# Kernel tuning notes

Measured on AMD Instinct MI355X. Metric: run time of the kernel, lower is better.

## Reference

```python
import math
import jax, jax.numpy as jnp
import numpy as np

V, D, H, L, F, S, B = 32000, 768, 12, 6, 3072, 2048, 4
DK = D // H


def setup_inputs() -> dict:
    key = jax.random.key(0)
    ks = jax.random.split(key, 16)
    sc = 0.02
    n = jax.random.normal
    inp = {
        "input_ids": jax.random.randint(ks[0], (B, S), 0, V, dtype=jnp.int64)
        if jax.config.jax_enable_x64 else jax.random.randint(ks[0], (B, S), 0, V, dtype=jnp.int32),
        "emb": n(ks[1], (V, D), jnp.float32) * sc,
        "Wq": n(ks[2], (L, D, D), jnp.float32) * sc, "bq": jnp.zeros((L, D), jnp.float32),
        "Wk": n(ks[3], (L, D, D), jnp.float32) * sc, "bk": jnp.zeros((L, D), jnp.float32),
        "Wv": n(ks[4], (L, D, D), jnp.float32) * sc, "bv": jnp.zeros((L, D), jnp.float32),
        "Wo": n(ks[5], (L, D, D), jnp.float32) * sc, "bo": jnp.zeros((L, D), jnp.float32),
        "W1": n(ks[6], (L, D, F), jnp.float32) * sc, "b1": jnp.zeros((L, F), jnp.float32),
        "W2": n(ks[7], (L, F, D), jnp.float32) * sc, "b2": jnp.zeros((L, D), jnp.float32),
        "gamma": jnp.ones((L, D), jnp.float32), "beta": jnp.zeros((L, D), jnp.float32),
    }
    return inp


def _pos_encoding(seq_len, d):
    pos = jnp.arange(seq_len, dtype=jnp.float32)[:, None]                  # [S,1]
    div = jnp.exp(jnp.arange(0, d, 2, dtype=jnp.float32) * (-math.log(10000.0) / d))
    ang = pos * div                                                        # [S,D/2]
    return jnp.stack([jnp.sin(ang), jnp.cos(ang)], axis=-1).reshape(seq_len, d)


def _layernorm(x, g, b, eps=1e-5):
    mu = x.mean(-1, keepdims=True)
    var = ((x - mu) ** 2).mean(-1, keepdims=True)
    return (x - mu) * jax.lax.rsqrt(var + eps) * g + b


def _forward(input_ids, emb, Wq, bq, Wk, bk, Wv, bv, Wo, bo, W1, b1, W2, b2, gamma, beta):
    mask = (input_ids != 1)[:, None, None, :]                              # [B,1,1,S]
    x = emb[input_ids] + _pos_encoding(input_ids.shape[1], emb.shape[1])   # [B,S,D]

    def layer(x, p):
        wq, bq_, wk, bk_, wv, bv_, wo, bo_, w1, b1_, w2, b2_, g, bt = p
        def heads(h):  # [B,S,D] -> [B,H,S,DK]
            return h.reshape(B, S, H, DK).transpose(0, 2, 1, 3)
        q = heads(x @ wq + bq_)
        k = heads(x @ wk + bk_)
        v = heads(x @ wv + bv_)
        scores = jnp.einsum("bhqd,bhkd->bhqk", q, k) / math.sqrt(DK)
        scores = jnp.where(mask, scores, -1e9)
        attn = jax.nn.softmax(scores, axis=-1)
        o = jnp.einsum("bhqk,bhkd->bhqd", attn, v)
        o = o.transpose(0, 2, 1, 3).reshape(B, S, D) @ wo + bo_
        x1 = _layernorm(x + o, g, bt)
        ff = jax.nn.relu(x1 @ w1 + b1_) @ w2 + b2_
        return _layernorm(x1 + ff, g, bt), None  # same norm params reused (as in source)

    x, _ = jax.lax.scan(layer, x, (Wq, bq, Wk, bk, Wv, bv, Wo, bo, W1, b1, W2, b2, gamma, beta))
    return x.mean(axis=1)                                                  # [B,D]


def reference(input_ids, emb, Wq, bq, Wk, bk, Wv, bv, Wo, bo, W1, b1, W2, b2, gamma, beta):
    return _forward(input_ids, emb, Wq, bq, Wk, bk, Wv, bv, Wo, bo, W1, b1, W2, b2, gamma, beta)
```

## Files before the change

### kernel.cpp

```cpp
#include <hip/hip_runtime.h>
#include <hip/hip_bf16.h>
#include <math.h>

typedef unsigned short u16;
typedef unsigned long long u64;
using bf16x8 = __attribute__((ext_vector_type(8))) short;
using f32x4  = __attribute__((ext_vector_type(4))) float;

static constexpr int kD = 768;
static constexpr int kH = 12;
static constexpr int kL = 6;
static constexpr int kF = 3072;
static constexpr int kS = 2048;
static constexpr int kB = 4;
static constexpr int kQW = 2304;
static constexpr int kNT = kB * kS;

static constexpr float kQScale = 0.18033688011112043f;

__device__ __forceinline__ u16 f2bf(float f) {
    return __bfloat16_as_ushort(__float2bfloat16(f));
}
__device__ __forceinline__ float b2f(u16 u) {
    return __uint_as_float((unsigned)u << 16);
}
__device__ __forceinline__ unsigned cvtpk(float a, float b) {
    unsigned d;
    asm volatile("v_cvt_pk_bf16_f32 %0, %1, %2" : "=v"(d) : "v"(a), "v"(b));
    return d;
}
__device__ __forceinline__ float exp2fast(float x) {
#if __has_builtin(__builtin_amdgcn_exp2f)
    return __builtin_amdgcn_exp2f(x);
#else
    return __expf(x * 0.6931471805599453f);
#endif
}

__device__ __forceinline__ void gload16(const void* g, void* l) {
    auto gp = reinterpret_cast<const __attribute__((address_space(1))) unsigned int*>(
        reinterpret_cast<uintptr_t>(g));
    auto lp = reinterpret_cast<__attribute__((address_space(3))) unsigned int*>(
        reinterpret_cast<uintptr_t>(l));
    __builtin_amdgcn_global_load_lds(gp, lp, 16, 0, 0);
}

__global__ __launch_bounds__(256) void embed_pe(
    const int* __restrict__ ids, const float* __restrict__ emb,
    u16* __restrict__ xbf)
{
    const int t = blockIdx.x;
    const int s = t & (kS - 1);
    const int id = ids[t];
#pragma unroll
    for (int j = 0; j < 3; ++j) {
        const int d = threadIdx.x + (j << 8);
        const float i2 = (float)((d >> 1) << 1);
        const float dv = __expf(i2 * (-9.210340371976184f / 768.f));
        const float ang = (float)s * dv;
        const float pe = (d & 1) ? cosf(ang) : sinf(ang);
        xbf[(size_t)t * kD + d] = f2bf(emb[(size_t)id * kD + d] + pe);
    }
}

__global__ __launch_bounds__(256) void embed_pe_f32(
    const int* __restrict__ ids, const float* __restrict__ emb,
    float* __restrict__ x)
{
    const int t = blockIdx.x;
    const int s = t & (kS - 1);
    const int id = ids[t];
#pragma unroll
    for (int j = 0; j < 3; ++j) {
        const int d = threadIdx.x + (j << 8);
        const float i2 = (float)((d >> 1) << 1);
        const float dv = __expf(i2 * (-9.210340371976184f / 768.f));
        const float ang = (float)s * dv;
        const float pe = (d & 1) ? cosf(ang) : sinf(ang);
        x[(size_t)t * kD + d] = emb[(size_t)id * kD + d] + pe;
    }
}

__global__ __launch_bounds__(64) void mk_maskbits(const int* __restrict__ ids,
                                                  u64* __restrict__ mbits)
{
    const int w = blockIdx.x;
    const int lane = threadIdx.x;
    const u64 m = __ballot(ids[(size_t)w * 64 + lane] != 1);
    if (lane == 0) mbits[w] = m;
}

__global__ __launch_bounds__(256) void bias_build(
    const float* __restrict__ bq, const float* __restrict__ bk,
    const float* __restrict__ bv, const float* __restrict__ bo,
    const float* __restrict__ b1, const float* __restrict__ b2,
    float* __restrict__ ba)
{
    const int i = blockIdx.x * 256 + threadIdx.x;
    if (i >= 6 * 6912) return;
    const int l = i / 6912, p = i % 6912;
    float v;
    if      (p < 768)  v = bq[l * 768 + p] * kQScale;
    else if (p < 1536) v = bk[l * 768 + p - 768];
    else if (p < 2304) v = bv[l * 768 + p - 1536];
    else if (p < 3072) v = bo[l * 768 + p - 2304];
    else if (p < 6144) v = b1[(size_t)l * 3072 + p - 3072];
    else               v = b2[l * 768 + p - 6144];
    ba[i] = v;
}

static constexpr size_t OFF_WO = (size_t)2304 * 768;
static constexpr size_t OFF_W1 = OFF_WO + (size_t)768 * 768;
static constexpr size_t OFF_W2 = OFF_W1 + (size_t)3072 * 768;
static constexpr size_t WARENA_E = OFF_W2 + (size_t)768 * 3072;

__global__ __launch_bounds__(256) void cvt_all(
    const float* __restrict__ Wq, const float* __restrict__ Wk,
    const float* __restrict__ Wv, const float* __restrict__ Wo,
    const float* __restrict__ W1, const float* __restrict__ W2,
    u16* __restrict__ wa)
{
    __shared__ float T[64][68];
    const int t = blockIdx.x;
    const float* S; u16* Dp; int Nsrc, Kdst, srow0, scol0; float sc = 1.f;
    if (t < 432) {
        const int ni = t % 36, ki = t / 36;
        const int ng = ni * 64;
        const int sel = ng / 768;
        scol0 = ng % 768; srow0 = ki * 64;
        S = (sel == 0) ? Wq : (sel == 1) ? Wk : Wv;
        if (sel == 0) sc = kQScale;
        Nsrc = 768; Kdst = 768;
        Dp = wa + (size_t)ng * 768 + srow0;
    } else if (t < 576) {
        const int tt = t - 432; const int ni = tt % 12, ki = tt / 12;
        scol0 = ni * 64; srow0 = ki * 64;
        S = Wo; Nsrc = 768; Kdst = 768;
        Dp = wa + OFF_WO + (size_t)(ni * 64) * 768 + srow0;
    } else if (t < 1152) {
        const int tt = t - 576; const int ni = tt % 48, ki = tt / 48;
        scol0 = ni * 64; srow0 = ki * 64;
        S = W1; Nsrc = 3072; Kdst = 768;
        Dp = wa + OFF_W1 + (size_t)(ni * 64) * 768 + srow0;
    } else {
        const int tt = t - 1152; const int ni = tt % 12, ki = tt / 12;
        scol0 = ni * 64; srow0 = ki * 64;
        S = W2; Nsrc = 768; Kdst = 3072;
        Dp = wa + OFF_W2 + (size_t)(ni * 64) * 3072 + srow0;
    }
    const int tid = threadIdx.x;
#pragma unroll
    for (int i = 0; i < 4; ++i) {
        const int idx = tid + (i << 8);
        const int kr = idx >> 4;
        const int nc = (idx & 15) << 2;
        const float4 v = *(const float4*)(S + (size_t)(srow0 + kr) * Nsrc + scol0 + nc);
        T[kr][nc] = v.x; T[kr][nc + 1] = v.y; T[kr][nc + 2] = v.z; T[kr][nc + 3] = v.w;
    }
    __syncthreads();
#pragma unroll
    for (int i = 0; i < 4; ++i) {
        const int idx = tid + (i << 8);
        const int nr = idx >> 4;
        const int kc = (idx & 15) << 2;
        ushort4 o;
        o.x = f2bf(T[kc][nr] * sc);     o.y = f2bf(T[kc + 1][nr] * sc);
        o.z = f2bf(T[kc + 2][nr] * sc); o.w = f2bf(T[kc + 3][nr] * sc);
        *(ushort4*)(Dp + (size_t)nr * Kdst + kc) = o;
    }
}

__global__ __launch_bounds__(512, 1) void gemm256(
    const u16* __restrict__ A, const u16* __restrict__ Bt,
    const float* __restrict__ bias, void* __restrict__ Cv,
    u16* __restrict__ vTp, int M, int N, int K, int mode)
{
    __shared__ u16 As[3][8192];
    __shared__ u16 Bs[3][8192];
    const int tid = threadIdx.x;
    const int l = tid & 63;
    const int lo = l & 15, hi = l >> 4;
    const int w = tid >> 6, wr = w >> 2, wc = w & 3;

    int brow = blockIdx.x, bcol = blockIdx.y;
    const int gx = gridDim.x;
    if ((gx & 7) == 0) {
        const int id = blockIdx.y * gx + blockIdx.x;
        const int xcd = id & 7, idx = id >> 3;
        const int rpx = gx >> 3;
        brow = xcd * rpx + (idx % rpx);
        bcol = idx / rpx;
    }
    const size_t row0 = (size_t)brow * 256;
    const size_t col0 = (size_t)bcol * 256;

    const int c0 = tid, c1 = tid + 512;
    const int r0 = c0 >> 2, g0 = (c0 & 3) ^ ((r0 >> 1) & 3);
    const int r1 = c1 >> 2, g1 = (c1 & 3) ^ ((r1 >> 1) & 3);
    const u16* a0 = A  + (row0 + r0) * K + g0 * 8;
    const u16* a1 = A  + (row0 + r1) * K + g1 * 8;
    const u16* b0 = Bt + (col0 + r0) * K + g0 * 8;
    const u16* b1 = Bt + (col0 + r1) * K + g1 * 8;

    f32x4 acc[8][4];
#pragma unroll
    for (int i = 0; i < 8; ++i)
#pragma unroll
        for (int j = 0; j < 4; ++j)
#pragma unroll
            for (int r = 0; r < 4; ++r) acc[i][j][r] = 0.f;

    int aoff[8], boff[4];
#pragma unroll
    for (int i = 0; i < 8; ++i) {
        const int ra = wr * 128 + i * 16 + lo;
        aoff[i] = ra * 32 + ((hi ^ ((ra >> 1) & 3)) << 3);
    }
#pragma unroll
    for (int j = 0; j < 4; ++j) {
        const int rb = wc * 64 + j * 16 + lo;
        boff[j] = rb * 32 + ((hi ^ ((rb >> 1) & 3)) << 3);
    }

    const int NT = K >> 5;
#pragma unroll
    for (int t = 0; t < 2; ++t) {
        const int k0 = t << 5;
        gload16(a0 + k0, As[t] + c0 * 8);
        gload16(a1 + k0, As[t] + c1 * 8);
        gload16(b0 + k0, Bs[t] + c0 * 8);
        gload16(b1 + k0, Bs[t] + c1 * 8);
    }

    int cur = 0;
    for (int t = 0; t < NT; ++t) {
        if (t + 1 < NT) {
            asm volatile("s_waitcnt vmcnt(8)" ::: "memory");
        } else {
            asm volatile("s_waitcnt vmcnt(0)" ::: "memory");
        }
        __builtin_amdgcn_s_barrier();
        if (t + 2 < NT) {
            const int k0 = (t + 2) << 5;
            const int nb = (cur + 2 >= 3) ? cur - 1 : cur + 2;
            gload16(a0 + k0, As[nb] + c0 * 8);
            gload16(a1 + k0, As[nb] + c1 * 8);
            gload16(b0 + k0, Bs[nb] + c0 * 8);
            gload16(b1 + k0, Bs[nb] + c1 * 8);
        }
        bf16x8 af[8], bfr[4];
#pragma unroll
        for (int i = 0; i < 8; ++i) af[i]  = *(const bf16x8*)&As[cur][aoff[i]];
#pragma unroll
        for (int j = 0; j < 4; ++j) bfr[j] = *(const bf16x8*)&Bs[cur][boff[j]];
        __builtin_amdgcn_s_setprio(1);
#pragma unroll
        for (int i = 0; i < 8; ++i)
#pragma unroll
            for (int j = 0; j < 4; ++j)
                acc[i][j] = __builtin_amdgcn_mfma_f32_16x16x32_bf16(
                    af[i], bfr[j], acc[i][j], 0, 0, 0);
        __builtin_amdgcn_s_setprio(0);
        cur = (cur + 1 == 3) ? 0 : cur + 1;
    }

    const bool vmode = (mode == 3) && (col0 >= 1536);
    if (vmode) {
#pragma unroll
        for (int i = 0; i < 8; ++i) {
            const size_t rbase = row0 + wr * 128 + i * 16 + hi * 4;
            const size_t tb = (rbase >> 6) * 64;
            const int k0 = (int)(rbase & 63);
            const int pos = (((k0 >> 2) & 3) << 3) + (((k0 >> 4) & 1) << 2)
                          + ((k0 >> 5) << 5);
#pragma unroll
            for (int j = 0; j < 4; ++j) {
                const size_t c = col0 + wc * 64 + j * 16 + lo;
                const float bs = bias[c];
                const size_t d = c - 1536;
                ushort4 o;
                o.x = f2bf(acc[i][j][0] + bs);
                o.y = f2bf(acc[i][j][1] + bs);
                o.z = f2bf(acc[i][j][2] + bs);
                o.w = f2bf(acc[i][j][3] + bs);
                *(ushort4*)(vTp + d * (size_t)M + tb + pos) = o;
            }
        }
        return;
    }

#pragma unroll
    for (int i = 0; i < 8; ++i) {
        const size_t rbase = row0 + wr * 128 + i * 16 + hi * 4;
#pragma unroll
        for (int j = 0; j < 4; ++j) {
            const size_t c = col0 + wc * 64 + j * 16 + lo;
            const float bs = bias[c];
#pragma unroll
            for (int r = 0; r < 4; ++r) {
                float v = acc[i][j][r] + bs;
                if (mode == 2) v = fmaxf(v, 0.f);
                ((u16*)Cv)[(rbase + r) * (size_t)N + c] = f2bf(v);
            }
        }
    }
}

__global__ __launch_bounds__(256) void gemm_bf16(
    const u16* __restrict__ A, const u16* __restrict__ Bt,
    const float* __restrict__ bias, void* __restrict__ Cv,
    u16* __restrict__ vTp, int M, int N, int K, int mode)
{
    __shared__ u16 As[2][4096];
    __shared__ u16 Bs[2][4096];
    const int tid = threadIdx.x;
    const int l = tid & 63;
    const int lo = l & 15, hi = l >> 4;
    const int w = tid >> 6, wr = w >> 1, wc = w & 1;

    int brow = blockIdx.x, bcol = blockIdx.y;
    const int gx = gridDim.x;
    if ((gx & 7) == 0) {
        const int id = blockIdx.y * gx + blockIdx.x;
        const int xcd = id & 7, idx = id >> 3;
        const int rpx = gx >> 3;
        brow = xcd * rpx + (idx % rpx);
        bcol = idx / rpx;
    }
    const size_t row0 = (size_t)brow * 128;
    const size_t col0 = (size_t)bcol * 128;

    const int c0 = tid, c1 = tid + 256;
    const int r0 = c0 >> 2, g0 = (c0 & 3) ^ ((r0 >> 1) & 3);
    const int r1 = c1 >> 2, g1 = (c1 & 3) ^ ((r1 >> 1) & 3);
    const u16* a0 = A  + (row0 + r0) * K + g0 * 8;
    const u16* a1 = A  + (row0 + r1) * K + g1 * 8;
    const u16* b0 = Bt + (col0 + r0) * K + g0 * 8;
    const u16* b1 = Bt + (col0 + r1) * K + g1 * 8;

    f32x4 acc[4][4];
#pragma unroll
    for (int i = 0; i < 4; ++i)
#pragma unroll
        for (int j = 0; j < 4; ++j)
#pragma unroll
            for (int r = 0; r < 4; ++r) acc[i][j][r] = 0.f;

    int aoff[4], boff[4];
#pragma unroll
    for (int i = 0; i < 4; ++i) {
        const int ra = wr * 64 + i * 16 + lo;
        aoff[i] = ra * 32 + ((hi ^ ((ra >> 1) & 3)) << 3);
        const int rb = wc * 64 + i * 16 + lo;
        boff[i] = rb * 32 + ((hi ^ ((rb >> 1) & 3)) << 3);
    }

    const int NT = K >> 5;
    gload16(a0, As[0] + c0 * 8);
    gload16(a1, As[0] + c1 * 8);
    gload16(b0, Bs[0] + c0 * 8);
    gload16(b1, Bs[0] + c1 * 8);

    int cur = 0;
    for (int t = 0; t < NT; ++t) {
        if (t + 1 < NT) {
            const int k0 = (t + 1) << 5;
            const int nb = cur ^ 1;
            gload16(a0 + k0, As[nb] + c0 * 8);
            gload16(a1 + k0, As[nb] + c1 * 8);
            gload16(b0 + k0, Bs[nb] + c0 * 8);
            gload16(b1 + k0, Bs[nb] + c1 * 8);
            asm volatile("s_waitcnt vmcnt(4)" ::: "memory");
        } else {
            asm volatile("s_waitcnt vmcnt(0)" ::: "memory");
        }
        __builtin_amdgcn_s_barrier();
        bf16x8 af[4], bfr[4];
#pragma unroll
        for (int i = 0; i < 4; ++i) af[i]  = *(const bf16x8*)&As[cur][aoff[i]];
#pragma unroll
        for (int j = 0; j < 4; ++j) bfr[j] = *(const bf16x8*)&Bs[cur][boff[j]];
#pragma unroll
        for (int i = 0; i < 4; ++i)
#pragma unroll
            for (int j = 0; j < 4; ++j)
                acc[i][j] = __builtin_amdgcn_mfma_f32_16x16x32_bf16(
                    af[i], bfr[j], acc[i][j], 0, 0, 0);
        asm volatile("s_waitcnt lgkmcnt(0)" ::: "memory");
        __builtin_amdgcn_sched_barrier(0);
        __builtin_amdgcn_s_barrier();
        cur ^= 1;
    }

#pragma unroll
    for (int i = 0; i < 4; ++i) {
        const size_t rbase = row0 + wr * 64 + i * 16 + hi * 4;
#pragma unroll
        for (int j = 0; j < 4; ++j) {
            const size_t c = col0 + wc * 64 + j * 16 + lo;
            const float bs = bias[c];
#pragma unroll
            for (int r = 0; r < 4; ++r) {
                float v = acc[i][j][r] + bs;
                if (mode == 2) v = fmaxf(v, 0.f);
                ((u16*)Cv)[(rbase + r) * (size_t)N + c] = f2bf(v);
            }
        }
    }
}

__global__ __launch_bounds__(512) void attn_mfma(
    const u16* __restrict__ QKV, const u16* __restrict__ vT,
    const u64* __restrict__ mbits, u16* __restrict__ O)
{
    __shared__ u16 Ks[2][4096];
    __shared__ u16 Vs[2][4096];

    const int tid = threadIdx.x, l = tid & 63, w = tid >> 6;
    const int lo = l & 15, hi = l >> 4;

    const int flat = blockIdx.x + 16 * (blockIdx.y + 12 * blockIdx.z);
    const int nf = (flat & 7) * 96 + (flat >> 3);
    const int qi = nf & 15;
    const int h  = (nf >> 4) % 12;
    const int b  = nf / 192;
    const int q0 = qi << 7;

    bf16x8 qf0, qf1;
    {
        const u16* qp = QKV + ((size_t)(b * kS + q0 + w * 16 + lo)) * kQW
                            + h * 64 + hi * 8;
        qf0 = *(const bf16x8*)qp;
        qf1 = *(const bf16x8*)(qp + 32);
    }

    const int rw = tid >> 3, sx = tid & 7, E = sx ^ (rw & 7);
    const u16* Kbase = QKV + (size_t)(b * kS) * kQW + 768 + h * 64;
    const u16* Vbase = vT + (size_t)(h * 64) * kNT + b * kS;

    f32x4 accO[4];
#pragma unroll
    for (int n = 0; n < 4; ++n)
#pragma unroll
        for (int r = 0; r < 4; ++r) accO[n][r] = 0.f;
    float m = -3.0e38f, lsum = 0.f;

    const int ksw = (lo & 7) << 3;
    constexpr int NTt = kS / 64;

    gload16(Kbase + (size_t)rw * kQW + E * 8, Ks[0] + tid * 8);
    gload16(Vbase + (size_t)rw * kNT + E * 8, Vs[0] + tid * 8);

    int cur = 0;
    for (int kt = 0; kt < NTt; ++kt) {
        asm volatile("s_waitcnt vmcnt(0)" ::: "memory");
        __syncthreads();

        if (kt + 1 < NTt) {
            const size_t kof = (size_t)((kt + 1) << 6) * kQW;
            const size_t vof = (size_t)((kt + 1) << 6);
            gload16(Kbase + kof + (size_t)rw * kQW + E * 8, Ks[cur ^ 1] + tid * 8);
            gload16(Vbase + (size_t)rw * kNT + vof + E * 8, Vs[cur ^ 1] + tid * 8);
        }

        f32x4 st[4];
        __builtin_amdgcn_s_setprio(1);
#pragma unroll
        for (int j = 0; j < 4; ++j) {
#pragma unroll
            for (int r = 0; r < 4; ++r) st[j][r] = 0.f;
            const int kb2 = (j * 16 + lo) * 64;
            const bf16x8 k0 = *(const bf16x8*)&Ks[cur][kb2 + ((hi * 8)      ^ ksw)];
            const bf16x8 k1 = *(const bf16x8*)&Ks[cur][kb2 + ((hi * 8 + 32) ^ ksw)];
            st[j] = __builtin_amdgcn_mfma_f32_16x16x32_bf16(k0, qf0, st[j], 0, 0, 0);
            st[j] = __builtin_amdgcn_mfma_f32_16x16x32_bf16(k1, qf1, st[j], 0, 0, 0);
        }
        __builtin_amdgcn_s_setprio(0);

        float rmax = st[0][0];
#pragma unroll
        for (int j = 0; j < 4; ++j)
#pragma unroll
            for (int r = 0; r < 4; ++r) rmax = fmaxf(rmax, st[j][r]);
        rmax = fmaxf(rmax, __shfl_xor(rmax, 16));
        rmax = fmaxf(rmax, __shfl_xor(rmax, 32));

        const bool skip = __all(rmax <= m + 11.0f);
        if (!skip) {
            const float mn = fmaxf(m, rmax);
            const float corr = exp2fast(m - mn);
            m = mn;
            lsum *= corr;
            float c2[4];
#pragma unroll
            for (int r = 0; r < 4; ++r) c2[r] = __shfl(corr, hi * 4 + r);
#pragma unroll
            for (int n = 0; n < 4; ++n)
#pragma unroll
                for (int r = 0; r < 4; ++r) accO[n][r] *= c2[r];
        }

#pragma unroll
        for (int j = 0; j < 4; ++j)
#pragma unroll
            for (int r = 0; r < 4; ++r) st[j][r] = exp2fast(st[j][r] - m);

        const u64 mb = mbits[b * 32 + kt];
        if (mb != ~0ull) {
#pragma unroll
            for (int j = 0; j < 4; ++j)
#pragma unroll
                for (int r = 0; r < 4; ++r)
                    if (!((mb >> (j * 16 + hi * 4 + r)) & 1)) st[j][r] = 0.f;
        }

        float ts = 0.f;
#pragma unroll
        for (int j = 0; j < 4; ++j)
#pragma unroll
            for (int r = 0; r < 4; ++r) ts += st[j][r];
        ts += __shfl_xor(ts, 16);
        ts += __shfl_xor(ts, 32);
        lsum += ts;

        union PU { unsigned u[4]; bf16x8 v; } p0, p1;
        p0.u[0] = cvtpk(st[0][0], st[0][1]); p0.u[1] = cvtpk(st[0][2], st[0][3]);
        p0.u[2] = cvtpk(st[1][0], st[1][1]); p0.u[3] = cvtpk(st[1][2], st[1][3]);
        p1.u[0] = cvtpk(st[2][0], st[2][1]); p1.u[1] = cvtpk(st[2][2], st[2][3]);
        p1.u[2] = cvtpk(st[3][0], st[3][1]); p1.u[3] = cvtpk(st[3][2], st[3][3]);

        __builtin_amdgcn_s_setprio(1);
#pragma unroll
        for (int n = 0; n < 4; ++n) {
            const int vb2 = (n * 16 + lo) * 64;
            const bf16x8 v0 = *(const bf16x8*)&Vs[cur][vb2 + ((hi * 8)      ^ ksw)];
            const bf16x8 v1 = *(const bf16x8*)&Vs[cur][vb2 + ((hi * 8 + 32) ^ ksw)];
            accO[n] = __builtin_amdgcn_mfma_f32_16x16x32_bf16(p0.v, v0, accO[n], 0, 0, 0);
            accO[n] = __builtin_amdgcn_mfma_f32_16x16x32_bf16(p1.v, v1, accO[n], 0, 0, 0);
        }
        __builtin_amdgcn_s_setprio(0);
        cur ^= 1;
    }

    float linv[4];
#pragma unroll
    for (int r = 0; r < 4; ++r) linv[r] = 1.f / __shfl(lsum, hi * 4 + r);
#pragma unroll
    for (int n = 0; n < 4; ++n)
#pragma unroll
        for (int r = 0; r < 4; ++r)
            O[((size_t)(b * kS + q0 + w * 16 + hi * 4 + r)) * kD
              + h * 64 + n * 16 + lo] = f2bf(accO[n][r] * linv[r]);
}

__global__ __launch_bounds__(256) void add_ln_bf(
    const u16* __restrict__ a, const u16* __restrict__ r,
    const float* __restrict__ g, const float* __restrict__ bt,
    u16* __restrict__ out)
{
    const int lane = threadIdx.x & 63;
    const size_t row = (size_t)blockIdx.x * 4 + (threadIdx.x >> 6);
    const ushort4* a4 = (const ushort4*)(a + row * kD);
    const ushort4* r4 = (const ushort4*)(r + row * kD);
    float v[3][4];
    float s = 0.f;
#pragma unroll
    for (int j = 0; j < 3; ++j) {
        const ushort4 av = a4[j * 64 + lane];
        const ushort4 rv = r4[j * 64 + lane];
        v[j][0] = b2f(av.x) + b2f(rv.x);
        v[j][1] = b2f(av.y) + b2f(rv.y);
        v[j][2] = b2f(av.z) + b2f(rv.z);
        v[j][3] = b2f(av.w) + b2f(rv.w);
        s += v[j][0] + v[j][1] + v[j][2] + v[j][3];
    }
#pragma unroll
    for (int off = 32; off; off >>= 1) s += __shfl_xor(s, off);
    const float mu = s * (1.f / 768.f);
    float vs = 0.f;
#pragma unroll
    for (int j = 0; j < 3; ++j)
#pragma unroll
        for (int e = 0; e < 4; ++e) {
            const float t0 = v[j][e] - mu;
            vs = fmaf(t0, t0, vs);
        }
#pragma unroll
    for (int off = 32; off; off >>= 1) vs += __shfl_xor(vs, off);
    const float rstd = rsqrtf(vs * (1.f / 768.f) + 1e-5f);
    const float4* g4 = (const float4*)g;
    const float4* b4 = (const float4*)bt;
#pragma unroll
    for (int j = 0; j < 3; ++j) {
        const float4 gv = g4[j * 64 + lane];
        const float4 bv = b4[j * 64 + lane];
        ushort4 o;
        o.x = f2bf((v[j][0] - mu) * rstd * gv.x + bv.x);
        o.y = f2bf((v[j][1] - mu) * rstd * gv.y + bv.y);
        o.z = f2bf((v[j][2] - mu) * rstd * gv.z + bv.z);
        o.w = f2bf((v[j][3] - mu) * rstd * gv.w + bv.w);
        ((ushort4*)(out + row * kD))[j * 64 + lane] = o;
    }
}

__global__ __launch_bounds__(192) void mean_part_bf(
    const u16* __restrict__ x, float* __restrict__ mred)
{
    const int c = blockIdx.x, b = blockIdx.y;
    const int d = threadIdx.x * 4;
    const u16* base = x + ((size_t)b * kS + c * 32) * kD + d;
    float s0 = 0.f, s1 = 0.f, s2 = 0.f, s3 = 0.f;
#pragma unroll 8
    for (int t = 0; t < 32; ++t) {
        const ushort4 u = *(const ushort4*)(base + (size_t)t * kD);
        s0 += b2f(u.x); s1 += b2f(u.y); s2 += b2f(u.z); s3 += b2f(u.w);
    }
    float4 o; o.x = s0; o.y = s1; o.z = s2; o.w = s3;
    *(float4*)(mred + ((size_t)b * 64 + c) * kD + d) = o;
}

__global__ __launch_bounds__(256) void mean_fin(
    const float* __restrict__ mred, float* __restrict__ out)
{
    const int d = blockIdx.x * 256 + threadIdx.x;
    const int b = blockIdx.y;
    float s = 0.f;
#pragma unroll
    for (int c = 0; c < 64; ++c) s += mred[((size_t)b * 64 + c) * kD + d];
    out[b * kD + d] = s * (1.f / 2048.f);
}

__global__ __launch_bounds__(256) void add_ln_f32(
    const float* __restrict__ a, const float* __restrict__ r,
    const float* __restrict__ g, const float* __restrict__ bt,
    float* __restrict__ out)
{
    const int lane = threadIdx.x & 63;
    const size_t row = (size_t)blockIdx.x * 4 + (threadIdx.x >> 6);
    const float4* a4 = (const float4*)(a + row * kD);
    const float4* r4 = (const float4*)(r + row * kD);
    float4 v[3];
    float s = 0.f;
#pragma unroll
    for (int j = 0; j < 3; ++j) {
        const float4 av = a4[j * 64 + lane];
        const float4 rv = r4[j * 64 + lane];
        v[j].x = av.x + rv.x; v[j].y = av.y + rv.y;
        v[j].z = av.z + rv.z; v[j].w = av.w + rv.w;
        s += v[j].x + v[j].y + v[j].z + v[j].w;
    }
#pragma unroll
    for (int off = 32; off; off >>= 1) s += __shfl_xor(s, off);
    const float mu = s * (1.f / 768.f);
    float vs = 0.f;
#pragma unroll
    for (int j = 0; j < 3; ++j) {
        float t0 = v[j].x - mu, t1 = v[j].y - mu, t2 = v[j].z - mu, t3 = v[j].w - mu;
        vs = fmaf(t0, t0, fmaf(t1, t1, fmaf(t2, t2, fmaf(t3, t3, vs))));
    }
#pragma unroll
    for (int off = 32; off; off >>= 1) vs += __shfl_xor(vs, off);
    const float rstd = rsqrtf(vs * (1.f / 768.f) + 1e-5f);
    const float4* g4 = (const float4*)g;
    const float4* b4 = (const float4*)bt;
#pragma unroll
    for (int j = 0; j < 3; ++j) {
        const float4 gv = g4[j * 64 + lane];
        const float4 bv = b4[j * 64 + lane];
        float4 o;
        o.x = (v[j].x - mu) * rstd * gv.x + bv.x;
        o.y = (v[j].y - mu) * rstd * gv.y + bv.y;
        o.z = (v[j].z - mu) * rstd * gv.z + bv.z;
        o.w = (v[j].w - mu) * rstd * gv.w + bv.w;
        ((float4*)(out + row * kD))[j * 64 + lane] = o;
    }
}

__global__ __launch_bounds__(256) void mean_s(
    const float* __restrict__ x, float* __restrict__ out)
{
    const int d = blockIdx.x * 256 + threadIdx.x;
    const int b = blockIdx.y;
    float s = 0.f;
    for (int t = 0; t < kS; ++t) s += x[((size_t)b * kS + t) * kD + d];
    out[b * kD + d] = s * (1.f / 2048.f);
}

__global__ __launch_bounds__(256) void gemm_f32(
    const float* __restrict__ A, const float* __restrict__ W,
    const float* __restrict__ bias, float* __restrict__ C,
    int M, int N, int K, int relu)
{
    __shared__ float As[16][68];
    __shared__ float Bs[16][68];
    const int tid = threadIdx.x;
    const int row0 = blockIdx.x << 6;
    const int col0 = blockIdx.y << 6;
    const int tx = tid & 15, ty = tid >> 4;
    const int ar = tid >> 2;
    const int ak = (tid & 3) << 2;
    const int bk = tid >> 4;
    const int bc = (tid & 15) << 2;
    float acc[4][4] = {};
    const float* Ap = A + (size_t)(row0 + ar) * K + ak;
    const float* Wp = W + (size_t)bk * N + col0 + bc;
    for (int k0 = 0; k0 < K; k0 += 16) {
        const float4 a4 = *(const float4*)(Ap + k0);
        const float4 b4 = *(const float4*)(Wp + (size_t)k0 * N);
        __syncthreads();
        As[ak + 0][ar] = a4.x; As[ak + 1][ar] = a4.y;
        As[ak + 2][ar] = a4.z; As[ak + 3][ar] = a4.w;
        *(float4*)&Bs[bk][bc] = b4;
        __syncthreads();
#pragma unroll
        for (int kk = 0; kk < 16; ++kk) {
            const float4 av = *(const float4*)&As[kk][ty << 2];
            const float4 bv = *(const float4*)&Bs[kk][tx << 2];
            const float aa[4] = {av.x, av.y, av.z, av.w};
            const float bb[4] = {bv.x, bv.y, bv.z, bv.w};
#pragma unroll
            for (int i = 0; i < 4; ++i)
#pragma unroll
                for (int j = 0; j < 4; ++j)
                    acc[i][j] = fmaf(aa[i], bb[j], acc[i][j]);
        }
    }
#pragma unroll
    for (int i = 0; i < 4; ++i) {
        const int row = row0 + (ty << 2) + i;
#pragma unroll
        for (int j = 0; j < 4; ++j) {
            const int col = col0 + (tx << 2) + j;
            float v = acc[i][j] + bias[col];
            if (relu) v = fmaxf(v, 0.f);
            C[(size_t)row * N + col] = v;
        }
    }
}

__global__ __launch_bounds__(256) void attn_fused(
    const float* __restrict__ Q, const float* __restrict__ Km,
    const float* __restrict__ Vm, const int* __restrict__ ids,
    float* __restrict__ O)
{
    __shared__ float Ksf[64 * 64];
    __shared__ float Vtf[64 * 64];
    __shared__ float Qs[16][64];
    __shared__ float Psf[4][4][64];
    const int tid = threadIdx.x;
    const int w = tid >> 6;
    const int lane = tid & 63;
    const int h = blockIdx.y, b = blockIdx.z;
    const int qrow0 = blockIdx.x << 4;
    {
        const int r = tid >> 4;
        const int c4 = tid & 15;
        const float4 q4 = *(const float4*)(
            Q + ((size_t)(b * kS + qrow0 + r)) * kD + h * 64 + (c4 << 2));
        Qs[r][(c4 << 2) + 0] = q4.x * 0.125f;
        Qs[r][(c4 << 2) + 1] = q4.y * 0.125f;
        Qs[r][(c4 << 2) + 2] = q4.z * 0.125f;
        Qs[r][(c4 << 2) + 3] = q4.w * 0.125f;
    }
    float m[4], lsum[4], o[4];
#pragma unroll
    for (int r = 0; r < 4; ++r) { m[r] = -3.0e38f; lsum[r] = 0.f; o[r] = 0.f; }
    for (int kt = 0; kt < kS / 64; ++kt) {
        __syncthreads();
#pragma unroll
        for (int i = 0; i < 4; ++i) {
            const int lin = tid + (i << 8);
            const int row = lin >> 4;
            const int s4 = lin & 15;
            const size_t gro = ((size_t)(b * kS + (kt << 6) + row)) * kD + h * 64 + (s4 << 2);
            const float4 k4 = *(const float4*)(Km + gro);
            ((float4*)Ksf)[(row << 4) + (s4 ^ (row & 7))] = k4;
            const float4 v4 = *(const float4*)(Vm + gro);
            const int ksl = row >> 2, ke = row & 3;
            const int d0 = s4 << 2;
            Vtf[(d0 + 0) * 64 + ((ksl ^ ((d0 + 0) & 7)) << 2) + ke] = v4.x;
            Vtf[(d0 + 1) * 64 + ((ksl ^ ((d0 + 1) & 7)) << 2) + ke] = v4.y;
            Vtf[(d0 + 2) * 64 + ((ksl ^ ((d0 + 2) & 7)) << 2) + ke] = v4.z;
            Vtf[(d0 + 3) * 64 + ((ksl ^ ((d0 + 3) & 7)) << 2) + ke] = v4.w;
        }
        __syncthreads();
        const bool masked = (ids[(size_t)b * kS + (kt << 6) + lane] == 1);
        float scr[4] = {0.f, 0.f, 0.f, 0.f};
#pragma unroll
        for (int i16 = 0; i16 < 16; ++i16) {
            const float4 kv = ((const float4*)Ksf)[(lane << 4) + (i16 ^ (lane & 7))];
#pragma unroll
            for (int r = 0; r < 4; ++r) {
                const float4 qv = *(const float4*)&Qs[(w << 2) + r][i16 << 2];
                scr[r] = fmaf(kv.x, qv.x, fmaf(kv.y, qv.y,
                          fmaf(kv.z, qv.z, fmaf(kv.w, qv.w, scr[r]))));
            }
        }
#pragma unroll
        for (int r = 0; r < 4; ++r) {
            float sm = masked ? -3.0e38f : scr[r];
#pragma unroll
            for (int off = 32; off; off >>= 1) sm = fmaxf(sm, __shfl_xor(sm, off));
            const float mn = fmaxf(m[r], sm);
            const float cr = __expf(m[r] - mn);
            const float pv = masked ? 0.f : __expf(scr[r] - mn);
            float ps = pv;
#pragma unroll
            for (int off = 32; off; off >>= 1) ps += __shfl_xor(ps, off);
            lsum[r] = lsum[r] * cr + ps;
            o[r] *= cr;
            m[r] = mn;
            Psf[w][r][lane] = pv;
        }
#pragma unroll
        for (int i16 = 0; i16 < 16; ++i16) {
            const float4 vv = ((const float4*)Vtf)[(lane << 4) + (i16 ^ (lane & 7))];
#pragma unroll
            for (int r = 0; r < 4; ++r) {
                const float4 pv = *(const float4*)&Psf[w][r][i16 << 2];
                o[r] = fmaf(pv.x, vv.x, fmaf(pv.y, vv.y,
                        fmaf(pv.z, vv.z, fmaf(pv.w, vv.w, o[r]))));
            }
        }
    }
#pragma unroll
    for (int r = 0; r < 4; ++r)
        O[((size_t)(b * kS + qrow0 + (w << 2) + r)) * kD + h * 64 + lane] =
            o[r] / lsum[r];
}

extern "C" void kernel_launch(void* const* d_in, const int* in_sizes, int n_in,
                              void* d_out, int out_size, void* d_ws, size_t ws_size,
                              hipStream_t stream)
{
    const int*   ids   = (const int*)  d_in[0];
    const float* emb   = (const float*)d_in[1];
    const float* Wq    = (const float*)d_in[2];
    const float* bq    = (const float*)d_in[3];
    const float* Wk    = (const float*)d_in[4];
    const float* bk    = (const float*)d_in[5];
    const float* Wv    = (const float*)d_in[6];
    const float* bv    = (const float*)d_in[7];
    const float* Wo    = (const float*)d_in[8];
    const float* bo    = (const float*)d_in[9];
    const float* W1    = (const float*)d_in[10];
    const float* b1    = (const float*)d_in[11];
    const float* W2    = (const float*)d_in[12];
    const float* b2    = (const float*)d_in[13];
    const float* gamma = (const float*)d_in[14];
    const float* beta  = (const float*)d_in[15];
    float* out = (float*)d_out;

    const size_t BUFE = (size_t)kB * kS * kD;
    const size_t WDD  = (size_t)kD * kD;
    const size_t WDF  = (size_t)kD * kF;
    const size_t HIDE = (size_t)kB * kS * kF;
    const int NTOK = kB * kS;

    const size_t NEED = BUFE * 2 * 4
                      + HIDE * 2
                      + WARENA_E * 2
                      + (size_t)6 * 6912 * 4
                      + 128 * 8
                      + (size_t)kB * 64 * kD * 4;

    if (ws_size >= NEED) {
        u16*   xb  = (u16*)d_ws;
        u16*   x1b = xb + BUFE;
        u16*   ao  = x1b + BUFE;
        u16*   ob  = ao + BUFE;
        u16*   sc  = ob + BUFE;
        u16*   vtb = sc + (size_t)NTOK * kQW;
        u16*   wa  = sc + HIDE;
        float* ba  = (float*)(wa + WARENA_E);
        u64*   mbt = (u64*)(ba + 6 * 6912);
        float* mrd = (float*)(mbt + 128);

        embed_pe<<<NTOK, 256, 0, stream>>>(ids, emb, xb);
        mk_maskbits<<<kB * kS / 64, 64, 0, stream>>>(ids, mbt);
        bias_build<<<(6 * 6912 + 255) / 256, 256, 0, stream>>>(
            bq, bk, bv, bo, b1, b2, ba);

        for (int l = 0; l < kL; ++l) {
            const size_t oDD = (size_t)l * WDD;
            const size_t oDF = (size_t)l * WDF;
            const float* bl = ba + (size_t)l * 6912;
            const float* gl  = gamma + (size_t)l * kD;
            const float* btl = beta  + (size_t)l * kD;

            cvt_all<<<1728, 256, 0, stream>>>(
                Wq + oDD, Wk + oDD, Wv + oDD, Wo + oDD, W1 + oDF, W2 + oDF, wa);

            gemm256<<<dim3(32, 9), 512, 0, stream>>>(
                xb, wa, bl, sc, vtb, NTOK, kQW, kD, 3);

            attn_mfma<<<dim3(kS / 128, kH, kB), 512, 0, stream>>>(
                sc, vtb, mbt, ao);

            gemm_bf16<<<dim3(64, 6), 256, 0, stream>>>(
                ao, wa + OFF_WO, bl + 2304, ob, nullptr, NTOK, kD, kD, 1);

            add_ln_bf<<<NTOK / 4, 256, 0, stream>>>(xb, ob, gl, btl, x1b);

            gemm256<<<dim3(32, 12), 512, 0, stream>>>(
                x1b, wa + OFF_W1, bl + 3072, sc, nullptr, NTOK, kF, kD, 2);
            gemm_bf16<<<dim3(64, 6), 256, 0, stream>>>(
                sc, wa + OFF_W2, bl + 6144, ob, nullptr, NTOK, kD, kF, 1);

            add_ln_bf<<<NTOK / 4, 256, 0, stream>>>(x1b, ob, gl, btl, xb);
        }

        mean_part_bf<<<dim3(64, kB), 192, 0, stream>>>(xb, mrd);
        mean_fin<<<dim3(kD / 256, kB), 256, 0, stream>>>(mrd, out);
        return;
    }

    if (ws_size < 5 * BUFE * sizeof(float)) return;
    float* xb = (float*)d_ws;
    float* kb = xb + BUFE;
    float* qb = kb + BUFE;
    float* vb = qb + BUFE;
    float* obf = vb + BUFE;
    float* hb = qb;

    embed_pe_f32<<<NTOK, 256, 0, stream>>>(ids, emb, xb);
    for (int l = 0; l < kL; ++l) {
        const size_t oDD = (size_t)l * WDD;
        const size_t oDF = (size_t)l * WDF;
        gemm_f32<<<dim3(NTOK / 64, kD / 64), 256, 0, stream>>>(
            xb, Wq + oDD, bq + (size_t)l * kD, qb, NTOK, kD, kD, 0);
        gemm_f32<<<dim3(NTOK / 64, kD / 64), 256, 0, stream>>>(
            xb, Wk + oDD, bk + (size_t)l * kD, kb, NTOK, kD, kD, 0);
        gemm_f32<<<dim3(NTOK / 64, kD / 64), 256, 0, stream>>>(
            xb, Wv + oDD, bv + (size_t)l * kD, vb, NTOK, kD, kD, 0);
        attn_fused<<<dim3(kS / 16, kH, kB), 256, 0, stream>>>(qb, kb, vb, ids, obf);
        gemm_f32<<<dim3(NTOK / 64, kD / 64), 256, 0, stream>>>(
            obf, Wo + oDD, bo + (size_t)l * kD, qb, NTOK, kD, kD, 0);
        add_ln_f32<<<NTOK / 4, 256, 0, stream>>>(xb, qb,
            gamma + (size_t)l * kD, beta + (size_t)l * kD, kb);
        for (int c = 0; c < 2; ++c) {
            const size_t ro = (size_t)c * 4096;
            gemm_f32<<<dim3(4096 / 64, kF / 64), 256, 0, stream>>>(
                kb + ro * kD, W1 + oDF, b1 + (size_t)l * kF, hb, 4096, kF, kD, 1);
            gemm_f32<<<dim3(4096 / 64, kD / 64), 256, 0, stream>>>(
                hb, W2 + oDF, b2 + (size_t)l * kD, obf + ro * kD, 4096, kD, kF, 0);
        }
        add_ln_f32<<<NTOK / 4, 256, 0, stream>>>(kb, obf,
            gamma + (size_t)l * kD, beta + (size_t)l * kD, xb);
    }
    mean_s<<<dim3(kD / 256, kB), 256, 0, stream>>>(xb, out);
}
```

Measured before the change: 1.612 ms.

## Shrink big GEMM tile to 128x256 with 256 threads, two blocks per CU

Replaces the 256x256, 512-thread, triple-buffered GEMM used for the QKV and FFN1 projections with a 128x256 tile, 256 threads and double buffering. Launch bounds allow two blocks per CU, and the grid doubles in the row dimension. The intent is more resident blocks per CU and better load balance across the GPU. The cost is lower per-block data reuse (B tiles are fetched twice as often in total) and a shallower prefetch pipeline with an extra barrier per k-step.

Result: faster. 1.521 ms (-5.6%).

```diff
diff --git a/kernel.cpp b/kernel.cpp
--- a/kernel.cpp
+++ b/kernel.cpp
@@ -170,17 +170,17 @@
     }
 }
 
-__global__ __launch_bounds__(512, 1) void gemm256(
+__global__ __launch_bounds__(256, 2) void gemm256b(
     const u16* __restrict__ A, const u16* __restrict__ Bt,
     const float* __restrict__ bias, void* __restrict__ Cv,
     u16* __restrict__ vTp, int M, int N, int K, int mode)
 {
-    __shared__ u16 As[3][8192];
-    __shared__ u16 Bs[3][8192];
+    __shared__ u16 As[2][4096];
+    __shared__ u16 Bs[2][8192];
     const int tid = threadIdx.x;
     const int l = tid & 63;
     const int lo = l & 15, hi = l >> 4;
-    const int w = tid >> 6, wr = w >> 2, wc = w & 3;
+    const int wc = tid >> 6;
 
     int brow = blockIdx.x, bcol = blockIdx.y;
     const int gx = gridDim.x;
@@ -191,16 +191,21 @@
         brow = xcd * rpx + (idx % rpx);
         bcol = idx / rpx;
     }
-    const size_t row0 = (size_t)brow * 256;
+    const size_t row0 = (size_t)brow * 128;
     const size_t col0 = (size_t)bcol * 256;
 
-    const int c0 = tid, c1 = tid + 512;
-    const int r0 = c0 >> 2, g0 = (c0 & 3) ^ ((r0 >> 1) & 3);
-    const int r1 = c1 >> 2, g1 = (c1 & 3) ^ ((r1 >> 1) & 3);
-    const u16* a0 = A  + (row0 + r0) * K + g0 * 8;
-    const u16* a1 = A  + (row0 + r1) * K + g1 * 8;
-    const u16* b0 = Bt + (col0 + r0) * K + g0 * 8;
-    const u16* b1 = Bt + (col0 + r1) * K + g1 * 8;
+    const int ca0 = tid, ca1 = tid + 256;
+    const int ra0 = ca0 >> 2, ga0 = (ca0 & 3) ^ ((ra0 >> 1) & 3);
+    const int ra1 = ca1 >> 2, ga1 = (ca1 & 3) ^ ((ra1 >> 1) & 3);
+    const u16* aP0 = A + (row0 + ra0) * K + ga0 * 8;
+    const u16* aP1 = A + (row0 + ra1) * K + ga1 * 8;
+    const u16* bP[4];
+#pragma unroll
+    for (int q = 0; q < 4; ++q) {
+        const int c = tid + (q << 8);
+        const int r = c >> 2, g = (c & 3) ^ ((r >> 1) & 3);
+        bP[q] = Bt + (col0 + r) * K + g * 8;
+    }
 
     f32x4 acc[8][4];
 #pragma unroll
@@ -213,7 +218,7 @@
     int aoff[8], boff[4];
 #pragma unroll
     for (int i = 0; i < 8; ++i) {
-        const int ra = wr * 128 + i * 16 + lo;
+        const int ra = i * 16 + lo;
         aoff[i] = ra * 32 + ((hi ^ ((ra >> 1) & 3)) << 3);
     }
 #pragma unroll
@@ -223,31 +228,26 @@
     }
 
     const int NT = K >> 5;
-#pragma unroll
-    for (int t = 0; t < 2; ++t) {
-        const int k0 = t << 5;
-        gload16(a0 + k0, As[t] + c0 * 8);
-        gload16(a1 + k0, As[t] + c1 * 8);
-        gload16(b0 + k0, Bs[t] + c0 * 8);
-        gload16(b1 + k0, Bs[t] + c1 * 8);
-    }
-
-    int cur = 0;
+    gload16(aP0, As[0] + ca0 * 8);
+    gload16(aP1, As[0] + ca1 * 8);
+#pragma unroll
+    for (int q = 0; q < 4; ++q) gload16(bP[q], Bs[0] + (tid + (q << 8)) * 8);
+
     for (int t = 0; t < NT; ++t) {
+        const int cur = t & 1;
         if (t + 1 < NT) {
-            asm volatile("s_waitcnt vmcnt(8)" ::: "memory");
+            const int k0 = (t + 1) << 5;
+            const int nb = cur ^ 1;
+            gload16(aP0 + k0, As[nb] + ca0 * 8);
+            gload16(aP1 + k0, As[nb] + ca1 * 8);
+#pragma unroll
+            for (int q = 0; q < 4; ++q)
+                gload16(bP[q] + k0, Bs[nb] + (tid + (q << 8)) * 8);
+            asm volatile("s_waitcnt vmcnt(6)" ::: "memory");
         } else {
             asm volatile("s_waitcnt vmcnt(0)" ::: "memory");
         }
         __builtin_amdgcn_s_barrier();
-        if (t + 2 < NT) {
-            const int k0 = (t + 2) << 5;
-            const int nb = (cur + 2 >= 3) ? cur - 1 : cur + 2;
-            gload16(a0 + k0, As[nb] + c0 * 8);
-            gload16(a1 + k0, As[nb] + c1 * 8);
-            gload16(b0 + k0, Bs[nb] + c0 * 8);
-            gload16(b1 + k0, Bs[nb] + c1 * 8);
-        }
         bf16x8 af[8], bfr[4];
 #pragma unroll
         for (int i = 0; i < 8; ++i) af[i]  = *(const bf16x8*)&As[cur][aoff[i]];
@@ -261,14 +261,16 @@
                 acc[i][j] = __builtin_amdgcn_mfma_f32_16x16x32_bf16(
                     af[i], bfr[j], acc[i][j], 0, 0, 0);
         __builtin_amdgcn_s_setprio(0);
-        cur = (cur + 1 == 3) ? 0 : cur + 1;
+        asm volatile("s_waitcnt lgkmcnt(0)" ::: "memory");
+        __builtin_amdgcn_sched_barrier(0);
+        __builtin_amdgcn_s_barrier();
     }
 
     const bool vmode = (mode == 3) && (col0 >= 1536);
     if (vmode) {
 #pragma unroll
         for (int i = 0; i < 8; ++i) {
-            const size_t rbase = row0 + wr * 128 + i * 16 + hi * 4;
+            const size_t rbase = row0 + i * 16 + hi * 4;
             const size_t tb = (rbase >> 6) * 64;
             const int k0 = (int)(rbase & 63);
             const int pos = (((k0 >> 2) & 3) << 3) + (((k0 >> 4) & 1) << 2)
@@ -291,7 +293,7 @@
 
 #pragma unroll
     for (int i = 0; i < 8; ++i) {
-        const size_t rbase = row0 + wr * 128 + i * 16 + hi * 4;
+        const size_t rbase = row0 + i * 16 + hi * 4;
 #pragma unroll
         for (int j = 0; j < 4; ++j) {
             const size_t c = col0 + wc * 64 + j * 16 + lo;
@@ -891,7 +893,7 @@
             cvt_all<<<1728, 256, 0, stream>>>(
                 Wq + oDD, Wk + oDD, Wv + oDD, Wo + oDD, W1 + oDF, W2 + oDF, wa);
 
-            gemm256<<<dim3(32, 9), 512, 0, stream>>>(
+            gemm256b<<<dim3(64, 9), 256, 0, stream>>>(
                 xb, wa, bl, sc, vtb, NTOK, kQW, kD, 3);
 
             attn_mfma<<<dim3(kS / 128, kH, kB), 512, 0, stream>>>(
@@ -902,7 +904,7 @@
 
             add_ln_bf<<<NTOK / 4, 256, 0, stream>>>(xb, ob, gl, btl, x1b);
 
-            gemm256<<<dim3(32, 12), 512, 0, stream>>>(
+            gemm256b<<<dim3(64, 12), 256, 0, stream>>>(
                 x1b, wa + OFF_W1, bl + 3072, sc, nullptr, NTOK, kF, kD, 2);
             gemm_bf16<<<dim3(64, 6), 256, 0, stream>>>(
                 sc, wa + OFF_W2, bl + 6144, ob, nullptr, NTOK, kD, kF, 1);
```
